# Kernel optimization log

Measured on AMD Instinct MI355X. Metric: run time of the kernel, lower is better.

The kernel has to match this reference:

```python
import jax, jax.numpy as jnp
import numpy as np

DIM = 512
MOVE_EMBED_DIM = 64
NUM_BUCKETS = 64
EMBED = 768
B = 8192
STEPS = 10


def setup_inputs() -> dict:
    key = jax.random.key(0)
    ks = jax.random.split(key, 16)
    def g(i, shape, scale=0.02):
        return jax.random.normal(ks[i], shape, jnp.float32) * scale
    return {
        "boards": jax.random.normal(ks[0], (STEPS, B, EMBED), jnp.float32),
        "flags": jax.random.randint(ks[1], (STEPS - 2, B), 0, 2).astype(bool),
        "themes": jax.random.randint(ks[2], (B,), 0, 10),
        "moves": jax.random.randint(ks[3], (B,), 0, NUM_BUCKETS),
        "start": jax.random.uniform(ks[4], (DIM,), jnp.float32),
        "red_w": g(5, (DIM, EMBED)), "red_b": jnp.zeros((DIM,), jnp.float32),
        "ca_w": g(6, (DIM, DIM)), "ca_b": jnp.zeros((DIM,), jnp.float32),
        "cb_w": g(7, (DIM, DIM)), "cb_b": jnp.zeros((DIM,), jnp.float32),
        "move_emb": g(8, (NUM_BUCKETS, MOVE_EMBED_DIM), 1.0),
        "fc1_w": g(9, (DIM, DIM + MOVE_EMBED_DIM)), "fc1_b": jnp.zeros((DIM,), jnp.float32),
        "fc2_w": g(10, (DIM, DIM)), "fc2_b": jnp.zeros((DIM,), jnp.float32),
        "fc3_w": g(11, (1024, DIM)), "fc3_b": jnp.zeros((1024,), jnp.float32),
        "fc4_w": g(12, (1024, 1024)), "fc4_b": jnp.zeros((1024,), jnp.float32),
        "fc5_w": g(13, (512, 1024)), "fc5_b": jnp.zeros((512,), jnp.float32),
        "out_w": g(14, (1, 512)), "out_b": jnp.zeros((1,), jnp.float32),
    }


def reference(boards, flags, themes, moves, start, red_w, red_b, ca_w, ca_b,
              cb_w, cb_b, move_emb, fc1_w, fc1_b, fc2_w, fc2_b, fc3_w, fc3_b,
              fc4_w, fc4_b, fc5_w, fc5_b, out_w, out_b):
    bsz = boards.shape[1]
    # boards[0:2] are never masked; boards[2:10] are zeroed where flags are False
    full_flags = jnp.concatenate([jnp.ones((2, bsz), bool), flags], axis=0)  # [10,B]
    emb = jnp.where(full_flags[:, :, None], boards, 0.0)                     # [10,B,E]
    # shared dim reducer + relu applied to all 10 positions at once
    e = jax.nn.relu(jnp.einsum('sbe,de->sbd', emb, red_w) + red_b)           # [10,B,DIM]
    # precompute combiner_b contribution for every step (batched GEMM)
    eb = jnp.einsum('sbd,kd->sbk', e, cb_w) + cb_b                           # [10,B,DIM]
    # combiner_a(start)+combiner_b(e0) == combiner_a(h0)+... with h0 = start broadcast
    h0 = jnp.broadcast_to(start, (bsz, DIM))
    def step(h, eb_t):
        return jnp.tanh(h @ ca_w.T + ca_b + eb_t), None
    h, _ = jax.lax.scan(step, h0, eb)                                        # [B,DIM]
    # dropout layers are identity in eval mode
    m = move_emb[moves]                                                      # [B,MOVE_EMBED_DIM]
    x = jax.nn.relu(jnp.concatenate([h, m], axis=-1) @ fc1_w.T + fc1_b)
    x = jax.nn.relu(x @ fc2_w.T + fc2_b)
    x = jax.nn.relu(x @ fc3_w.T + fc3_b)
    x = jax.nn.relu(x @ fc4_w.T + fc4_b)
    x = jax.nn.relu(x @ fc5_w.T + fc5_b)
    return x @ out_w.T + out_b                                               # [B,1]
```

## Files before the change

kernel.cpp:

```cpp
#include <hip/hip_runtime.h>
#include <math.h>

#define BATCH  8192
#define EMBED  768
#define DIMD   512
#define MEDIM  64
#define NSTEP  10

typedef __bf16 bf16x8 __attribute__((ext_vector_type(8)));
typedef float  f32x4  __attribute__((ext_vector_type(4)));

__device__ __forceinline__ void load16_lds(const void* g, void* l)
{
    auto* gp = (__attribute__((address_space(1))) char*)(uintptr_t)g;
    auto* lp = (__attribute__((address_space(3))) char*)(unsigned int)(uintptr_t)l;
    __builtin_amdgcn_global_load_lds(gp, lp, 16, 0, 0);
}

#define WAITV(n) asm volatile("s_waitcnt vmcnt(" #n ")" ::: "memory")

#define BN 128
#define BK 32

template<int ACT, bool ADDEB, bool GATHER, int BMT>
__global__ __launch_bounds__(256)
void gemm_bf16(const __bf16* __restrict__ A, const __bf16* __restrict__ Bt,
               const float* __restrict__ bias, const __bf16* __restrict__ add,
               const __bf16* __restrict__ me, const int* __restrict__ moves,
               __bf16* __restrict__ C, int M, int N, int K)
{
    constexpr int NG = (BMT + BN) / 16;
    constexpr int AG = BMT / 16;
    constexpr int MR = BMT / 32;
    constexpr int NC = NG / 4;

    __shared__ __bf16 lds[3][(BMT + BN) * BK];

    const int nwg  = gridDim.x * gridDim.y;
    const int orig = blockIdx.y * gridDim.x + blockIdx.x;
    const int cpx  = nwg >> 3;
    const int swz  = (orig & 7) * cpx + (orig >> 3);
    const int bx   = swz % gridDim.x;
    const int by   = swz / gridDim.x;

    const int tid  = threadIdx.x;
    const int wave = tid >> 6;
    const int lane = tid & 63;
    const int row0 = by * BMT;
    const int col0 = bx * BN;

    const int wr = (wave >> 1) * (BMT / 2);
    const int wc = (wave & 1) * 64;
    const int fr = lane & 15;
    const int q  = lane >> 4;

    const int srow = lane >> 2;
    const int skk  = (((lane & 3) ^ ((lane >> 3) & 3)) * 8);

    int mv[2] = {0, 0};
    if (GATHER) {
#pragma unroll
        for (int ci = 0; ci < 2; ++ci)
            mv[ci] = moves[row0 + (ci * 4 + wave) * 16 + srow];
    }

    auto stage = [&](int buf, int k0) {
#pragma unroll
        for (int ci = 0; ci < NC; ++ci) {
            const int c = ci * 4 + wave;
            const int r = c * 16 + srow;
            const __bf16* g;
            if (c < AG) {
                if (GATHER) {
                    g = (k0 < DIMD)
                        ? (A  + (size_t)(row0 + r) * DIMD + k0 + skk)
                        : (me + (size_t)mv[ci] * MEDIM + (k0 - DIMD) + skk);
                } else {
                    g = A + (size_t)(row0 + r) * K + k0 + skk;
                }
            } else {
                g = Bt + (size_t)(col0 + (r - BMT)) * K + k0 + skk;
            }
            load16_lds(g, &lds[buf][c * 512]);
        }
    };

    auto frag = [&](const __bf16* base, int r) -> bf16x8 {
        return *(const bf16x8*)&base[r * 32 + ((q ^ ((r >> 1) & 3)) << 3)];
    };

    f32x4 acc[MR][4] = {};

    const int NT = K / BK;
    stage(0, 0);
    stage(1, BK);

    int rd = 0;
    for (int t = 0; t < NT; ++t) {
        if (t + 2 < NT) {
            int wrb = rd + 2; if (wrb >= 3) wrb -= 3;
            stage(wrb, (t + 2) * BK);
        }
        const int infl = (NT - 1 - t >= 2) ? 2 : (NT - 1 - t);
        if constexpr (NC == 4) {
            if (infl == 2)      WAITV(8);
            else if (infl == 1) WAITV(4);
            else                WAITV(0);
        } else {
            if (infl == 2)      WAITV(6);
            else if (infl == 1) WAITV(3);
            else                WAITV(0);
        }
        __builtin_amdgcn_s_barrier();
        __builtin_amdgcn_sched_barrier(0);

        const __bf16* As = lds[rd];
        const __bf16* Bs = lds[rd] + BMT * BK;
        bf16x8 af[MR], bfr[4];
#pragma unroll
        for (int m = 0; m < MR; ++m)
            af[m] = frag(As, wr + m * 16 + fr);
#pragma unroll
        for (int n = 0; n < 4; ++n)
            bfr[n] = frag(Bs, wc + n * 16 + fr);
#pragma unroll
        for (int m = 0; m < MR; ++m)
#pragma unroll
            for (int n = 0; n < 4; ++n)
                acc[m][n] = __builtin_amdgcn_mfma_f32_16x16x32_bf16(
                                af[m], bfr[n], acc[m][n], 0, 0, 0);

        __builtin_amdgcn_s_barrier();
        __builtin_amdgcn_sched_barrier(0);
        ++rd; if (rd >= 3) rd -= 3;
    }

#pragma unroll
    for (int m = 0; m < MR; ++m) {
#pragma unroll
        for (int n = 0; n < 4; ++n) {
            const int cc = col0 + wc + n * 16 + fr;
            const float bb = bias[cc];
#pragma unroll
            for (int j = 0; j < 4; ++j) {
                const int rr = row0 + wr + m * 16 + (lane >> 4) * 4 + j;
                float v = acc[m][n][j] + bb;
                if (ADDEB) v += (float)add[(size_t)rr * N + cc];
                if (ACT == 1) v = fmaxf(v, 0.0f);
                if (ACT == 2) {
                    const float p = __expf(2.0f * v);
                    v = 1.0f - 2.0f / (p + 1.0f);
                }
                C[(size_t)rr * N + cc] = (__bf16)v;
            }
        }
    }
}

__global__ __launch_bounds__(256)
void cvt_boards_all(const float* __restrict__ src, const int* __restrict__ flags,
                    __bf16* __restrict__ dst)
{
    const int idx  = blockIdx.x * 256 + threadIdx.x;
    const int grow = idx / 96;
    const int s    = grow >> 13;
    const int b    = grow & 8191;
    float m = 1.0f;
    if (s >= 2) m = flags[(size_t)(s - 2) * BATCH + b] ? 1.0f : 0.0f;
    const float4 v0 = ((const float4*)src)[(size_t)idx * 2];
    const float4 v1 = ((const float4*)src)[(size_t)idx * 2 + 1];
    bf16x8 o;
    o[0] = (__bf16)(v0.x * m); o[1] = (__bf16)(v0.y * m);
    o[2] = (__bf16)(v0.z * m); o[3] = (__bf16)(v0.w * m);
    o[4] = (__bf16)(v1.x * m); o[5] = (__bf16)(v1.y * m);
    o[6] = (__bf16)(v1.z * m); o[7] = (__bf16)(v1.w * m);
    *(bf16x8*)(dst + (size_t)idx * 8) = o;
}

enum : int { W_RED = 0, W_CA = 393216, W_CB = 655360, W_FC1 = 917504,
             W_FC2 = 1212416, W_FC3 = 1474560, W_FC4 = 1998848,
             W_FC5 = 3047424, W_ME = 3571712, W_TOTAL = 3575808 };

__global__ __launch_bounds__(256)
void cvt_weights(const float* __restrict__ w0, const float* __restrict__ w1,
                 const float* __restrict__ w2, const float* __restrict__ w3,
                 const float* __restrict__ w4, const float* __restrict__ w5,
                 const float* __restrict__ w6, const float* __restrict__ w7,
                 const float* __restrict__ w8, __bf16* __restrict__ dst)
{
    const int idx = blockIdx.x * 256 + threadIdx.x;
    if (idx >= W_TOTAL / 8) return;
    const int e = idx * 8;
    const float* src; int off;
    if      (e < W_CA)  { src = w0; off = W_RED; }
    else if (e < W_CB)  { src = w1; off = W_CA; }
    else if (e < W_FC1) { src = w2; off = W_CB; }
    else if (e < W_FC2) { src = w3; off = W_FC1; }
    else if (e < W_FC3) { src = w4; off = W_FC2; }
    else if (e < W_FC4) { src = w5; off = W_FC3; }
    else if (e < W_FC5) { src = w6; off = W_FC4; }
    else if (e < W_ME)  { src = w7; off = W_FC5; }
    else                { src = w8; off = W_ME; }
    const float4 v0 = ((const float4*)(src + (e - off)))[0];
    const float4 v1 = ((const float4*)(src + (e - off)))[1];
    bf16x8 o;
    o[0] = (__bf16)v0.x; o[1] = (__bf16)v0.y; o[2] = (__bf16)v0.z; o[3] = (__bf16)v0.w;
    o[4] = (__bf16)v1.x; o[5] = (__bf16)v1.y; o[6] = (__bf16)v1.z; o[7] = (__bf16)v1.w;
    *(bf16x8*)(dst + (size_t)e) = o;
}

__global__ __launch_bounds__(256)
void gemv_start(const float* __restrict__ caw, const float* __restrict__ cab,
                const float* __restrict__ start, float* __restrict__ tmp)
{
    __shared__ float s[DIMD];
    for (int i = threadIdx.x; i < DIMD; i += 256) s[i] = start[i];
    __syncthreads();
    const int n = blockIdx.x * 256 + threadIdx.x;
    const float4* w = (const float4*)(caw + (size_t)n * DIMD);
    float acc = 0.0f;
#pragma unroll 8
    for (int k = 0; k < DIMD / 4; ++k) {
        const float4 wv = w[k];
        acc += wv.x * s[k * 4] + wv.y * s[k * 4 + 1] +
               wv.z * s[k * 4 + 2] + wv.w * s[k * 4 + 3];
    }
    tmp[n] = acc + cab[n];
}

__global__ __launch_bounds__(256)
void h1_init(const float* __restrict__ tmp, const __bf16* __restrict__ eb0,
             __bf16* __restrict__ h)
{
    const int idx = blockIdx.x * 256 + threadIdx.x;
    const int c8 = idx & 63;
    const bf16x8 e = ((const bf16x8*)eb0)[idx];
    bf16x8 o;
#pragma unroll
    for (int j = 0; j < 8; ++j) {
        const float v = tmp[c8 * 8 + j] + (float)e[j];
        const float p = __expf(2.0f * v);
        o[j] = (__bf16)(1.0f - 2.0f / (p + 1.0f));
    }
    ((bf16x8*)h)[idx] = o;
}

__global__ __launch_bounds__(256)
void out_head(const __bf16* __restrict__ x, const float* __restrict__ out_w,
              const float* __restrict__ out_b, float* __restrict__ out)
{
    const int wid  = threadIdx.x >> 6;
    const int lane = threadIdx.x & 63;
    const int row  = blockIdx.x * 4 + wid;
    const bf16x8 xv = *(const bf16x8*)(x + (size_t)row * DIMD + lane * 8);
    const float4 w0 = ((const float4*)out_w)[lane * 2];
    const float4 w1 = ((const float4*)out_w)[lane * 2 + 1];
    float s = (float)xv[0] * w0.x + (float)xv[1] * w0.y + (float)xv[2] * w0.z +
              (float)xv[3] * w0.w + (float)xv[4] * w1.x + (float)xv[5] * w1.y +
              (float)xv[6] * w1.z + (float)xv[7] * w1.w;
#pragma unroll
    for (int off = 32; off; off >>= 1) s += __shfl_down(s, off, 64);
    if (lane == 0) out[row] = s + out_b[0];
}

extern "C" void kernel_launch(void* const* d_in, const int* in_sizes, int n_in,
                              void* d_out, int out_size, void* d_ws, size_t ws_size,
                              hipStream_t stream)
{
    const float* boards  = (const float*)d_in[0];
    const int*   flags   = (const int*)  d_in[1];
    const int*   moves   = (const int*)  d_in[3];
    const float* start   = (const float*)d_in[4];
    const float* red_w   = (const float*)d_in[5];
    const float* red_b   = (const float*)d_in[6];
    const float* ca_w    = (const float*)d_in[7];
    const float* ca_b    = (const float*)d_in[8];
    const float* cb_w    = (const float*)d_in[9];
    const float* cb_b    = (const float*)d_in[10];
    const float* move_emb= (const float*)d_in[11];
    const float* fc1_w   = (const float*)d_in[12];
    const float* fc1_b   = (const float*)d_in[13];
    const float* fc2_w   = (const float*)d_in[14];
    const float* fc2_b   = (const float*)d_in[15];
    const float* fc3_w   = (const float*)d_in[16];
    const float* fc3_b   = (const float*)d_in[17];
    const float* fc4_w   = (const float*)d_in[18];
    const float* fc4_b   = (const float*)d_in[19];
    const float* fc5_w   = (const float*)d_in[20];
    const float* fc5_b   = (const float*)d_in[21];
    const float* out_w   = (const float*)d_in[22];
    const float* out_b   = (const float*)d_in[23];

    __bf16* wsb = (__bf16*)d_ws;
    __bf16* wpool  = wsb;
    __bf16* b_all  = wsb + 3575808;
    __bf16* e_all  = wsb + 66490368;
    __bf16* eb_all = wsb + 108433408;
    __bf16* hA     = wsb + 150376448;
    __bf16* hB     = wsb + 154570752;
    float*  tmpv   = (float*)(wsb + 158765056);
    __bf16* x1     = wsb + 159789056;
    __bf16* x2     = wsb + 163983360;
    __bf16* x3     = wsb + 168177664;
    __bf16* x4     = wsb + 176566272;
    __bf16* x5     = wsb + 184954880;

    const dim3 blk(256);

    cvt_weights<<<1746, blk, 0, stream>>>(red_w, ca_w, cb_w, fc1_w, fc2_w,
                                          fc3_w, fc4_w, fc5_w, move_emb, wpool);
    cvt_boards_all<<<30720, blk, 0, stream>>>(boards, flags, b_all);
    gemv_start<<<2, blk, 0, stream>>>(ca_w, ca_b, start, tmpv);

    gemm_bf16<1, false, false, 128><<<dim3(4, 640), blk, 0, stream>>>(
        b_all, wpool + W_RED, red_b, nullptr, nullptr, nullptr, e_all,
        NSTEP * BATCH, DIMD, EMBED);
    gemm_bf16<0, false, false, 128><<<dim3(4, 640), blk, 0, stream>>>(
        e_all, wpool + W_CB, cb_b, nullptr, nullptr, nullptr, eb_all,
        NSTEP * BATCH, DIMD, DIMD);

    h1_init<<<2048, blk, 0, stream>>>(tmpv, eb_all, hA);

    __bf16* hcur = hA;
    __bf16* hnxt = hB;
    for (int s = 1; s < NSTEP; ++s) {
        const __bf16* ebs = eb_all + (size_t)s * BATCH * DIMD;
        gemm_bf16<2, true, false, 64><<<dim3(4, 128), blk, 0, stream>>>(
            hcur, wpool + W_CA, ca_b, ebs, nullptr, nullptr, hnxt,
            BATCH, DIMD, DIMD);
        __bf16* t = hcur; hcur = hnxt; hnxt = t;
    }

    gemm_bf16<1, false, true, 128><<<dim3(4, 64), blk, 0, stream>>>(
        hcur, wpool + W_FC1, fc1_b, nullptr, wpool + W_ME, moves, x1,
        BATCH, DIMD, DIMD + MEDIM);
    gemm_bf16<1, false, false, 128><<<dim3(4, 64), blk, 0, stream>>>(
        x1, wpool + W_FC2, fc2_b, nullptr, nullptr, nullptr, x2, BATCH, DIMD, DIMD);
    gemm_bf16<1, false, false, 128><<<dim3(8, 64), blk, 0, stream>>>(
        x2, wpool + W_FC3, fc3_b, nullptr, nullptr, nullptr, x3, BATCH, 1024, DIMD);
    gemm_bf16<1, false, false, 128><<<dim3(8, 64), blk, 0, stream>>>(
        x3, wpool + W_FC4, fc4_b, nullptr, nullptr, nullptr, x4, BATCH, 1024, 1024);
    gemm_bf16<1, false, false, 128><<<dim3(4, 64), blk, 0, stream>>>(
        x4, wpool + W_FC5, fc5_b, nullptr, nullptr, nullptr, x5, BATCH, DIMD, 1024);

    out_head<<<BATCH / 4, blk, 0, stream>>>(x5, out_w, out_b, (float*)d_out);
}
```

Before: 443.1 us.

## Add 256x256-tile 512-thread GEMM with triple-buffered LDS for the two large batched GEMMs

Adds a new bf16 MFMA GEMM kernel with 256x256 output tiles, 8 waves per block, a three-deep async global-to-LDS pipeline, XOR-swizzled LDS layout and block-index swizzling. It replaces the 128x128-tile kernel for the dim-reducer and combiner_b GEMMs over all 10 steps. The larger tiles increase operand reuse and reduce global traffic per FLOP. In exchange, each wave holds 128 accumulator registers and each block uses 96KB of dynamic LDS, which may lower occupancy and gives only 640 blocks.

After: 460.1 us. 3.8% more time.

```diff
diff --git a/kernel.cpp b/kernel.cpp
--- a/kernel.cpp
+++ b/kernel.cpp
@@ -151,6 +151,108 @@
                     const float p = __expf(2.0f * v);
                     v = 1.0f - 2.0f / (p + 1.0f);
                 }
+                C[(size_t)rr * N + cc] = (__bf16)v;
+            }
+        }
+    }
+}
+
+template<int ACT>
+__global__ __launch_bounds__(512)
+void gemm512(const __bf16* __restrict__ A, const __bf16* __restrict__ Bt,
+             const float* __restrict__ bias, __bf16* __restrict__ C,
+             int M, int N, int K)
+{
+    extern __shared__ __bf16 dyn[];
+
+    const int nwg  = gridDim.x * gridDim.y;
+    const int orig = blockIdx.y * gridDim.x + blockIdx.x;
+    const int cpx  = nwg >> 3;
+    const int swz  = (orig & 7) * cpx + (orig >> 3);
+    const int bx   = swz % gridDim.x;
+    const int by   = swz / gridDim.x;
+
+    const int tid  = threadIdx.x;
+    const int wave = tid >> 6;
+    const int lane = tid & 63;
+    const int row0 = by * 256;
+    const int col0 = bx * 256;
+
+    const int wr = (wave >> 2) * 128;
+    const int wc = (wave & 3) * 64;
+    const int fr = lane & 15;
+    const int q  = lane >> 4;
+
+    const int srow = lane >> 2;
+    const int skk  = (((lane & 3) ^ ((lane >> 3) & 3)) * 8);
+
+    auto stage = [&](int buf, int k0) {
+#pragma unroll
+        for (int ci = 0; ci < 4; ++ci) {
+            const int c = ci * 8 + wave;
+            const int r = c * 16 + srow;
+            const __bf16* g = (c < 16)
+                ? (A  + (size_t)(row0 + r)         * K + k0 + skk)
+                : (Bt + (size_t)(col0 + (r - 256)) * K + k0 + skk);
+            load16_lds(g, &dyn[buf * 16384 + c * 512]);
+        }
+    };
+
+    auto frag = [&](const __bf16* base, int r) -> bf16x8 {
+        return *(const bf16x8*)&base[r * 32 + ((q ^ ((r >> 1) & 3)) << 3)];
+    };
+
+    f32x4 acc[8][4] = {};
+
+    const int NT = K / BK;
+    stage(0, 0);
+    stage(1, BK);
+
+    int rd = 0;
+    for (int t = 0; t < NT; ++t) {
+        if (t + 2 < NT) {
+            int wrb = rd + 2; if (wrb >= 3) wrb -= 3;
+            stage(wrb, (t + 2) * BK);
+        }
+        const int infl = (NT - 1 - t >= 2) ? 2 : (NT - 1 - t);
+        if (infl == 2)      WAITV(8);
+        else if (infl == 1) WAITV(4);
+        else                WAITV(0);
+        __builtin_amdgcn_s_barrier();
+        __builtin_amdgcn_sched_barrier(0);
+
+        const __bf16* As = dyn + rd * 16384;
+        const __bf16* Bs = As + 256 * 32;
+        bf16x8 af[8], bfr[4];
+#pragma unroll
+        for (int m = 0; m < 8; ++m)
+            af[m] = frag(As, wr + m * 16 + fr);
+#pragma unroll
+        for (int n = 0; n < 4; ++n)
+            bfr[n] = frag(Bs, wc + n * 16 + fr);
+#pragma unroll
+        for (int m = 0; m < 8; ++m)
+#pragma unroll
+            for (int n = 0; n < 4; ++n)
+                acc[m][n] = __builtin_amdgcn_mfma_f32_16x16x32_bf16(
+                                af[m], bfr[n], acc[m][n], 0, 0, 0);
+
+        __builtin_amdgcn_s_barrier();
+        __builtin_amdgcn_sched_barrier(0);
+        ++rd; if (rd >= 3) rd -= 3;
+    }
+
+#pragma unroll
+    for (int m = 0; m < 8; ++m) {
+#pragma unroll
+        for (int n = 0; n < 4; ++n) {
+            const int cc = col0 + wc + n * 16 + fr;
+            const float bb = bias[cc];
+#pragma unroll
+            for (int j = 0; j < 4; ++j) {
+                const int rr = row0 + wr + m * 16 + (lane >> 4) * 4 + j;
+                float v = acc[m][n][j] + bb;
+                if (ACT == 1) v = fmaxf(v, 0.0f);
                 C[(size_t)rr * N + cc] = (__bf16)v;
             }
         }
@@ -306,18 +408,17 @@
     __bf16* x5     = wsb + 184954880;
 
     const dim3 blk(256);
+    const size_t LDS512 = 3 * 16384 * sizeof(__bf16);
 
     cvt_weights<<<1746, blk, 0, stream>>>(red_w, ca_w, cb_w, fc1_w, fc2_w,
                                           fc3_w, fc4_w, fc5_w, move_emb, wpool);
     cvt_boards_all<<<30720, blk, 0, stream>>>(boards, flags, b_all);
     gemv_start<<<2, blk, 0, stream>>>(ca_w, ca_b, start, tmpv);
 
-    gemm_bf16<1, false, false, 128><<<dim3(4, 640), blk, 0, stream>>>(
-        b_all, wpool + W_RED, red_b, nullptr, nullptr, nullptr, e_all,
-        NSTEP * BATCH, DIMD, EMBED);
-    gemm_bf16<0, false, false, 128><<<dim3(4, 640), blk, 0, stream>>>(
-        e_all, wpool + W_CB, cb_b, nullptr, nullptr, nullptr, eb_all,
-        NSTEP * BATCH, DIMD, DIMD);
+    gemm512<1><<<dim3(2, 320), dim3(512), LDS512, stream>>>(
+        b_all, wpool + W_RED, red_b, e_all, NSTEP * BATCH, DIMD, EMBED);
+    gemm512<0><<<dim3(2, 320), dim3(512), LDS512, stream>>>(
+        e_all, wpool + W_CB, cb_b, eb_all, NSTEP * BATCH, DIMD, DIMD);
 
     h1_init<<<2048, blk, 0, stream>>>(tmpv, eb_all, hA);
 
```

## Interleave next-tile global loads with MFMA and merge prep kernels into one launch

Applied to the files above, without the earlier changes.

The GEMM main loop now waits for the current tile before issuing the prefetch of tile t+2. It then spreads those global-to-LDS loads across the per-row-fragment MFMA groups and raises wave priority during the compute. Separately, the board conversion, weight conversion and start GEMV kernels are merged into one launch with block-range dispatch. The goals are better overlap of loads with matrix math and fewer kernel launches. In exchange, the pipeline keeps only one tile in flight at the wait point, which could expose more load latency.

New measurement: 436.8 us. No clear change (-1.4%).

```diff
diff --git a/kernel.cpp b/kernel.cpp
--- a/kernel.cpp
+++ b/kernel.cpp
@@ -64,25 +64,26 @@
             mv[ci] = moves[row0 + (ci * 4 + wave) * 16 + srow];
     }
 
+    auto stage_one = [&](int buf, int k0, int ci) {
+        const int c = ci * 4 + wave;
+        const int r = c * 16 + srow;
+        const __bf16* g;
+        if (c < AG) {
+            if (GATHER) {
+                g = (k0 < DIMD)
+                    ? (A  + (size_t)(row0 + r) * DIMD + k0 + skk)
+                    : (me + (size_t)mv[ci] * MEDIM + (k0 - DIMD) + skk);
+            } else {
+                g = A + (size_t)(row0 + r) * K + k0 + skk;
+            }
+        } else {
+            g = Bt + (size_t)(col0 + (r - BMT)) * K + k0 + skk;
+        }
+        load16_lds(g, &lds[buf][c * 512]);
+    };
     auto stage = [&](int buf, int k0) {
 #pragma unroll
-        for (int ci = 0; ci < NC; ++ci) {
-            const int c = ci * 4 + wave;
-            const int r = c * 16 + srow;
-            const __bf16* g;
-            if (c < AG) {
-                if (GATHER) {
-                    g = (k0 < DIMD)
-                        ? (A  + (size_t)(row0 + r) * DIMD + k0 + skk)
-                        : (me + (size_t)mv[ci] * MEDIM + (k0 - DIMD) + skk);
-                } else {
-                    g = A + (size_t)(row0 + r) * K + k0 + skk;
-                }
-            } else {
-                g = Bt + (size_t)(col0 + (r - BMT)) * K + k0 + skk;
-            }
-            load16_lds(g, &lds[buf][c * 512]);
-        }
+        for (int ci = 0; ci < NC; ++ci) stage_one(buf, k0, ci);
     };
 
     auto frag = [&](const __bf16* base, int r) -> bf16x8 {
@@ -97,38 +98,40 @@
 
     int rd = 0;
     for (int t = 0; t < NT; ++t) {
-        if (t + 2 < NT) {
-            int wrb = rd + 2; if (wrb >= 3) wrb -= 3;
-            stage(wrb, (t + 2) * BK);
-        }
-        const int infl = (NT - 1 - t >= 2) ? 2 : (NT - 1 - t);
-        if constexpr (NC == 4) {
-            if (infl == 2)      WAITV(8);
-            else if (infl == 1) WAITV(4);
-            else                WAITV(0);
+        if (t + 1 < NT) {
+            if constexpr (NC == 4) WAITV(4); else WAITV(3);
         } else {
-            if (infl == 2)      WAITV(6);
-            else if (infl == 1) WAITV(3);
-            else                WAITV(0);
+            WAITV(0);
         }
         __builtin_amdgcn_s_barrier();
         __builtin_amdgcn_sched_barrier(0);
 
+        const bool dost = (t + 2 < NT);
+        int wrb = rd + 2; if (wrb >= 3) wrb -= 3;
+        const int k0s = (t + 2) * BK;
+
         const __bf16* As = lds[rd];
         const __bf16* Bs = lds[rd] + BMT * BK;
-        bf16x8 af[MR], bfr[4];
-#pragma unroll
-        for (int m = 0; m < MR; ++m)
-            af[m] = frag(As, wr + m * 16 + fr);
+        bf16x8 bfr[4];
 #pragma unroll
         for (int n = 0; n < 4; ++n)
             bfr[n] = frag(Bs, wc + n * 16 + fr);
-#pragma unroll
-        for (int m = 0; m < MR; ++m)
+
+        __builtin_amdgcn_s_setprio(1);
+#pragma unroll
+        for (int m = 0; m < MR; ++m) {
+            if (dost) {
+#pragma unroll
+                for (int ci = m * NC / MR; ci < (m + 1) * NC / MR; ++ci)
+                    stage_one(wrb, k0s, ci);
+            }
+            const bf16x8 af = frag(As, wr + m * 16 + fr);
 #pragma unroll
             for (int n = 0; n < 4; ++n)
                 acc[m][n] = __builtin_amdgcn_mfma_f32_16x16x32_bf16(
-                                af[m], bfr[n], acc[m][n], 0, 0, 0);
+                                af, bfr[n], acc[m][n], 0, 0, 0);
+        }
+        __builtin_amdgcn_s_setprio(0);
 
         __builtin_amdgcn_s_barrier();
         __builtin_amdgcn_sched_barrier(0);
@@ -157,75 +160,74 @@
     }
 }
 
-__global__ __launch_bounds__(256)
-void cvt_boards_all(const float* __restrict__ src, const int* __restrict__ flags,
-                    __bf16* __restrict__ dst)
-{
-    const int idx  = blockIdx.x * 256 + threadIdx.x;
-    const int grow = idx / 96;
-    const int s    = grow >> 13;
-    const int b    = grow & 8191;
-    float m = 1.0f;
-    if (s >= 2) m = flags[(size_t)(s - 2) * BATCH + b] ? 1.0f : 0.0f;
-    const float4 v0 = ((const float4*)src)[(size_t)idx * 2];
-    const float4 v1 = ((const float4*)src)[(size_t)idx * 2 + 1];
-    bf16x8 o;
-    o[0] = (__bf16)(v0.x * m); o[1] = (__bf16)(v0.y * m);
-    o[2] = (__bf16)(v0.z * m); o[3] = (__bf16)(v0.w * m);
-    o[4] = (__bf16)(v1.x * m); o[5] = (__bf16)(v1.y * m);
-    o[6] = (__bf16)(v1.z * m); o[7] = (__bf16)(v1.w * m);
-    *(bf16x8*)(dst + (size_t)idx * 8) = o;
-}
-
 enum : int { W_RED = 0, W_CA = 393216, W_CB = 655360, W_FC1 = 917504,
              W_FC2 = 1212416, W_FC3 = 1474560, W_FC4 = 1998848,
              W_FC5 = 3047424, W_ME = 3571712, W_TOTAL = 3575808 };
 
+#define NB_BOARDS 30720
+#define NB_W      1746
 __global__ __launch_bounds__(256)
-void cvt_weights(const float* __restrict__ w0, const float* __restrict__ w1,
-                 const float* __restrict__ w2, const float* __restrict__ w3,
-                 const float* __restrict__ w4, const float* __restrict__ w5,
-                 const float* __restrict__ w6, const float* __restrict__ w7,
-                 const float* __restrict__ w8, __bf16* __restrict__ dst)
-{
-    const int idx = blockIdx.x * 256 + threadIdx.x;
-    if (idx >= W_TOTAL / 8) return;
-    const int e = idx * 8;
-    const float* src; int off;
-    if      (e < W_CA)  { src = w0; off = W_RED; }
-    else if (e < W_CB)  { src = w1; off = W_CA; }
-    else if (e < W_FC1) { src = w2; off = W_CB; }
-    else if (e < W_FC2) { src = w3; off = W_FC1; }
-    else if (e < W_FC3) { src = w4; off = W_FC2; }
-    else if (e < W_FC4) { src = w5; off = W_FC3; }
-    else if (e < W_FC5) { src = w6; off = W_FC4; }
-    else if (e < W_ME)  { src = w7; off = W_FC5; }
-    else                { src = w8; off = W_ME; }
-    const float4 v0 = ((const float4*)(src + (e - off)))[0];
-    const float4 v1 = ((const float4*)(src + (e - off)))[1];
-    bf16x8 o;
-    o[0] = (__bf16)v0.x; o[1] = (__bf16)v0.y; o[2] = (__bf16)v0.z; o[3] = (__bf16)v0.w;
-    o[4] = (__bf16)v1.x; o[5] = (__bf16)v1.y; o[6] = (__bf16)v1.z; o[7] = (__bf16)v1.w;
-    *(bf16x8*)(dst + (size_t)e) = o;
-}
-
-__global__ __launch_bounds__(256)
-void gemv_start(const float* __restrict__ caw, const float* __restrict__ cab,
-                const float* __restrict__ start, float* __restrict__ tmp)
-{
-    __shared__ float s[DIMD];
-    for (int i = threadIdx.x; i < DIMD; i += 256) s[i] = start[i];
-    __syncthreads();
-    const int n = blockIdx.x * 256 + threadIdx.x;
-    const float4* w = (const float4*)(caw + (size_t)n * DIMD);
-    float acc = 0.0f;
+void prep(const float* __restrict__ boards, const int* __restrict__ flags,
+          __bf16* __restrict__ b_all,
+          const float* __restrict__ w0, const float* __restrict__ w1,
+          const float* __restrict__ w2, const float* __restrict__ w3,
+          const float* __restrict__ w4, const float* __restrict__ w5,
+          const float* __restrict__ w6, const float* __restrict__ w7,
+          const float* __restrict__ w8, __bf16* __restrict__ wpool,
+          const float* __restrict__ cab, const float* __restrict__ start,
+          float* __restrict__ tmp)
+{
+    const int bid = blockIdx.x;
+    if (bid < NB_BOARDS) {
+        const int idx  = bid * 256 + threadIdx.x;
+        const int grow = idx / 96;
+        const int s    = grow >> 13;
+        const int b    = grow & 8191;
+        float m = 1.0f;
+        if (s >= 2) m = flags[(size_t)(s - 2) * BATCH + b] ? 1.0f : 0.0f;
+        const float4 v0 = ((const float4*)boards)[(size_t)idx * 2];
+        const float4 v1 = ((const float4*)boards)[(size_t)idx * 2 + 1];
+        bf16x8 o;
+        o[0] = (__bf16)(v0.x * m); o[1] = (__bf16)(v0.y * m);
+        o[2] = (__bf16)(v0.z * m); o[3] = (__bf16)(v0.w * m);
+        o[4] = (__bf16)(v1.x * m); o[5] = (__bf16)(v1.y * m);
+        o[6] = (__bf16)(v1.z * m); o[7] = (__bf16)(v1.w * m);
+        *(bf16x8*)(b_all + (size_t)idx * 8) = o;
+    } else if (bid < NB_BOARDS + NB_W) {
+        const int idx = (bid - NB_BOARDS) * 256 + threadIdx.x;
+        if (idx >= W_TOTAL / 8) return;
+        const int e = idx * 8;
+        const float* src; int off;
+        if      (e < W_CA)  { src = w0; off = W_RED; }
+        else if (e < W_CB)  { src = w1; off = W_CA; }
+        else if (e < W_FC1) { src = w2; off = W_CB; }
+        else if (e < W_FC2) { src = w3; off = W_FC1; }
+        else if (e < W_FC3) { src = w4; off = W_FC2; }
+        else if (e < W_FC4) { src = w5; off = W_FC3; }
+        else if (e < W_FC5) { src = w6; off = W_FC4; }
+        else if (e < W_ME)  { src = w7; off = W_FC5; }
+        else                { src = w8; off = W_ME; }
+        const float4 v0 = ((const float4*)(src + (e - off)))[0];
+        const float4 v1 = ((const float4*)(src + (e - off)))[1];
+        bf16x8 o;
+        o[0] = (__bf16)v0.x; o[1] = (__bf16)v0.y; o[2] = (__bf16)v0.z; o[3] = (__bf16)v0.w;
+        o[4] = (__bf16)v1.x; o[5] = (__bf16)v1.y; o[6] = (__bf16)v1.z; o[7] = (__bf16)v1.w;
+        *(bf16x8*)(wpool + (size_t)e) = o;
+    } else {
+        __shared__ float s[DIMD];
+        for (int i = threadIdx.x; i < DIMD; i += 256) s[i] = start[i];
+        __syncthreads();
+        const int n = (bid - NB_BOARDS - NB_W) * 256 + threadIdx.x;
+        const float4* w = (const float4*)(w1 + (size_t)n * DIMD);
+        float acc = 0.0f;
 #pragma unroll 8
-    for (int k = 0; k < DIMD / 4; ++k) {
-        const float4 wv = w[k];
-        acc += wv.x * s[k * 4] + wv.y * s[k * 4 + 1] +
-               wv.z * s[k * 4 + 2] + wv.w * s[k * 4 + 3];
-    }
-    tmp[n] = acc + cab[n];
+        for (int k = 0; k < DIMD / 4; ++k) {
+            const float4 wv = w[k];
+            acc += wv.x * s[k * 4] + wv.y * s[k * 4 + 1] +
+                   wv.z * s[k * 4 + 2] + wv.w * s[k * 4 + 3];
+        }
+        tmp[n] = acc + cab[n];
+    }
 }
 
 __global__ __launch_bounds__(256)
@@ -307,10 +309,10 @@
 
     const dim3 blk(256);
 
-    cvt_weights<<<1746, blk, 0, stream>>>(red_w, ca_w, cb_w, fc1_w, fc2_w,
-                                          fc3_w, fc4_w, fc5_w, move_emb, wpool);
-    cvt_boards_all<<<30720, blk, 0, stream>>>(boards, flags, b_all);
-    gemv_start<<<2, blk, 0, stream>>>(ca_w, ca_b, start, tmpv);
+    prep<<<NB_BOARDS + NB_W + 2, blk, 0, stream>>>(
+        boards, flags, b_all,
+        red_w, ca_w, cb_w, fc1_w, fc2_w, fc3_w, fc4_w, fc5_w, move_emb, wpool,
+        ca_b, start, tmpv);
 
     gemm_bf16<1, false, false, 128><<<dim3(4, 640), blk, 0, stream>>>(
         b_all, wpool + W_RED, red_b, nullptr, nullptr, nullptr, e_all,
```
